# Performance work log

Measured on AMD Instinct MI355X. Metric: run time of the kernel, lower is better.

The kernel has to match this reference:

```python
import jax, jax.numpy as jnp
import numpy as np

A, B, K = 8192, 8192, 10

def setup_inputs() -> dict:
    key = jax.random.key(0)
    k1, k2, k3 = jax.random.split(key, 3)
    W = jax.random.uniform(k1, (A, B), dtype=jnp.float32)      # similarity weights (a,b)
    P_l = jax.random.uniform(k2, (A, K), dtype=jnp.float32)    # left cluster probs (a,k)
    P_r = jax.random.uniform(k3, (B, K), dtype=jnp.float32)    # right cluster probs (b,k)
    clusters_p = jnp.ones((K,), dtype=jnp.float32) / K         # nn.Parameter ones(k)/k
    return {"W": W, "P_l": P_l, "P_r": P_r, "clusters_p": clusters_p}

def reference(W, P_l, P_r, clusters_p):
    # Original math: sum_{a,b,k} W[a,b] * (P_l[a,k] + P_r[b,k] - 2*P_l[a,k]*P_r[b,k]) / clusters_p[k]
    # Decomposes exactly (no (a,b,k) intermediate):
    row_sum = W.sum(axis=1)                 # (a,)
    col_sum = W.sum(axis=0)                 # (b,)
    term_l = row_sum @ P_l                  # (k,)  sum_a rowsum[a] * P_l[a,k]
    term_r = col_sum @ P_r                  # (k,)  sum_b colsum[b] * P_r[b,k]
    WPr = W @ P_r                           # (a,k)
    cross = jnp.sum(P_l * WPr, axis=0)      # (k,)  diag(P_l^T W P_r)
    per_cluster = term_l + term_r - 2.0 * cross
    return jnp.sum(per_cluster / clusters_p)
```

## Files before the change

### kernel.cpp

```cpp
#include <hip/hip_runtime.h>


constexpr int K     = 10;
constexpr int TM    = 32;
constexpr int BLOCK = 256;
constexpr int TN    = BLOCK * 4;

__global__ void prcut_zero_out(float* out) {
    if (threadIdx.x == 0) out[0] = 0.0f;
}

__global__ __launch_bounds__(BLOCK) void prcut_main(
    const float* __restrict__ W,
    const float* __restrict__ Pl,
    const float* __restrict__ Pr,
    const float* __restrict__ cp,
    float* __restrict__ out,
    int Bn)
{
    float inv[K];
#pragma unroll
    for (int k = 0; k < K; ++k) inv[k] = 1.0f / cp[k];

    const int col4 = blockIdx.x * TN + threadIdx.x * 4;
    const int a0   = blockIdx.y * TM;

    float pr[4][K];
    float rs[4];
#pragma unroll
    for (int j = 0; j < 4; ++j) {
        const float* prp = Pr + (size_t)(col4 + j) * K;
        float s = 0.0f;
#pragma unroll
        for (int k = 0; k < K; ++k) {
            float v = prp[k] * inv[k];
            pr[j][k] = v;
            s += v;
        }
        rs[j] = s;
    }

    const float* wp = W + (size_t)a0 * Bn + col4;
    float acc = 0.0f;

#pragma unroll 4
    for (int r = 0; r < TM; ++r) {
        const float4 w = *reinterpret_cast<const float4*>(wp);
        wp += Bn;

        const float* plp = Pl + (size_t)(a0 + r) * K;
        float pl[K];
        float la = 0.0f;
#pragma unroll
        for (int k = 0; k < K; ++k) {
            pl[k] = plp[k];
            la = fmaf(pl[k], inv[k], la);
        }

        float d0 = 0.f, d1 = 0.f, d2 = 0.f, d3 = 0.f;
#pragma unroll
        for (int k = 0; k < K; ++k) {
            d0 = fmaf(pl[k], pr[0][k], d0);
            d1 = fmaf(pl[k], pr[1][k], d1);
            d2 = fmaf(pl[k], pr[2][k], d2);
            d3 = fmaf(pl[k], pr[3][k], d3);
        }

        const float c0 = fmaf(-2.0f, d0, la + rs[0]);
        const float c1 = fmaf(-2.0f, d1, la + rs[1]);
        const float c2 = fmaf(-2.0f, d2, la + rs[2]);
        const float c3 = fmaf(-2.0f, d3, la + rs[3]);

        acc = fmaf(w.x, c0, acc);
        acc = fmaf(w.y, c1, acc);
        acc = fmaf(w.z, c2, acc);
        acc = fmaf(w.w, c3, acc);
    }

#pragma unroll
    for (int off = 32; off > 0; off >>= 1)
        acc += __shfl_down(acc, off, 64);

    __shared__ float wsum[BLOCK / 64];
    const int lane = threadIdx.x & 63;
    const int wid  = threadIdx.x >> 6;
    if (lane == 0) wsum[wid] = acc;
    __syncthreads();

    if (threadIdx.x == 0) {
        float s = 0.0f;
#pragma unroll
        for (int i = 0; i < BLOCK / 64; ++i) s += wsum[i];
        atomicAdd(out, s);
    }
}

extern "C" void kernel_launch(void* const* d_in, const int* in_sizes, int n_in,
                              void* d_out, int out_size, void* d_ws, size_t ws_size,
                              hipStream_t stream) {
    const float* W  = (const float*)d_in[0];
    const float* Pl = (const float*)d_in[1];
    const float* Pr = (const float*)d_in[2];
    const float* cp = (const float*)d_in[3];
    float* out = (float*)d_out;

    const int Kn = in_sizes[3];
    const int A  = in_sizes[1] / Kn;
    const int B  = in_sizes[2] / Kn;

    prcut_zero_out<<<1, 64, 0, stream>>>(out);

    dim3 grid(B / TN, A / TM);
    prcut_main<<<grid, BLOCK, 0, stream>>>(W, Pl, Pr, cp, out, B);
}
```

Measured before the change: 378.8 us.

## Use full-row 1024-thread blocks with 8 columns per thread and nontemporal loads

Each block now covers a whole 16-row band of W, and each thread handles 8 columns split across the two halves of the row, so the Pr slices loaded into registers are reused across more W elements. The per-element coefficient is rewritten algebraically as la + sum_k pr_k*(1-2*pl_k), which drops the separate row-sum and the -2 fixups. W is read with nontemporal loads because it is streamed only once. Holding 80 pr values per thread in a 1024-thread block raises register pressure, and the grid is now one-dimensional with only 512 blocks, both of which can lower occupancy. The layout also assumes B equals 8*1024.

```diff
diff --git a/kernel.cpp b/kernel.cpp
--- a/kernel.cpp
+++ b/kernel.cpp
@@ -2,9 +2,10 @@
 
 
 constexpr int K     = 10;
-constexpr int TM    = 32;
-constexpr int BLOCK = 256;
-constexpr int TN    = BLOCK * 4;
+constexpr int TM    = 16;
+constexpr int BLOCK = 1024;
+
+typedef float f4 __attribute__((ext_vector_type(4)));
 
 __global__ void prcut_zero_out(float* out) {
     if (threadIdx.x == 0) out[0] = 0.0f;
@@ -22,59 +23,54 @@
 #pragma unroll
     for (int k = 0; k < K; ++k) inv[k] = 1.0f / cp[k];
 
-    const int col4 = blockIdx.x * TN + threadIdx.x * 4;
-    const int a0   = blockIdx.y * TM;
+    const int t    = threadIdx.x;
+    const int a0   = blockIdx.x * TM;
+    const int c0   = 4 * t;
+    const int half = Bn >> 1;
 
-    float pr[4][K];
-    float rs[4];
+    float pr[8][K];
 #pragma unroll
-    for (int j = 0; j < 4; ++j) {
-        const float* prp = Pr + (size_t)(col4 + j) * K;
-        float s = 0.0f;
+    for (int g = 0; g < 2; ++g) {
 #pragma unroll
-        for (int k = 0; k < K; ++k) {
-            float v = prp[k] * inv[k];
-            pr[j][k] = v;
-            s += v;
+        for (int j = 0; j < 4; ++j) {
+            const float* p = Pr + (size_t)(g * half + c0 + j) * K;
+#pragma unroll
+            for (int k = 0; k < K; ++k) pr[g * 4 + j][k] = p[k] * inv[k];
         }
-        rs[j] = s;
     }
 
-    const float* wp = W + (size_t)a0 * Bn + col4;
+    const float* wp = W + (size_t)a0 * Bn + c0;
     float acc = 0.0f;
 
-#pragma unroll 4
+#pragma unroll 2
     for (int r = 0; r < TM; ++r) {
-        const float4 w = *reinterpret_cast<const float4*>(wp);
+        const f4 w0 = __builtin_nontemporal_load(reinterpret_cast<const f4*>(wp));
+        const f4 w1 = __builtin_nontemporal_load(reinterpret_cast<const f4*>(wp + half));
         wp += Bn;
 
         const float* plp = Pl + (size_t)(a0 + r) * K;
-        float pl[K];
         float la = 0.0f;
+        float d[8];
+#pragma unroll
+        for (int j = 0; j < 8; ++j) d[j] = 0.0f;
+
 #pragma unroll
         for (int k = 0; k < K; ++k) {
-            pl[k] = plp[k];
-            la = fmaf(pl[k], inv[k], la);
+            const float plk = plp[k];
+            la = fmaf(plk, inv[k], la);
+            const float qk = fmaf(-2.0f, plk, 1.0f);
+#pragma unroll
+            for (int j = 0; j < 8; ++j) d[j] = fmaf(pr[j][k], qk, d[j]);
         }
 
-        float d0 = 0.f, d1 = 0.f, d2 = 0.f, d3 = 0.f;
-#pragma unroll
-        for (int k = 0; k < K; ++k) {
-            d0 = fmaf(pl[k], pr[0][k], d0);
-            d1 = fmaf(pl[k], pr[1][k], d1);
-            d2 = fmaf(pl[k], pr[2][k], d2);
-            d3 = fmaf(pl[k], pr[3][k], d3);
-        }
-
-        const float c0 = fmaf(-2.0f, d0, la + rs[0]);
-        const float c1 = fmaf(-2.0f, d1, la + rs[1]);
-        const float c2 = fmaf(-2.0f, d2, la + rs[2]);
-        const float c3 = fmaf(-2.0f, d3, la + rs[3]);
-
-        acc = fmaf(w.x, c0, acc);
-        acc = fmaf(w.y, c1, acc);
-        acc = fmaf(w.z, c2, acc);
-        acc = fmaf(w.w, c3, acc);
+        acc = fmaf(w0.x, la + d[0], acc);
+        acc = fmaf(w0.y, la + d[1], acc);
+        acc = fmaf(w0.z, la + d[2], acc);
+        acc = fmaf(w0.w, la + d[3], acc);
+        acc = fmaf(w1.x, la + d[4], acc);
+        acc = fmaf(w1.y, la + d[5], acc);
+        acc = fmaf(w1.z, la + d[6], acc);
+        acc = fmaf(w1.w, la + d[7], acc);
     }
 
 #pragma unroll
@@ -110,6 +106,5 @@
 
     prcut_zero_out<<<1, 64, 0, stream>>>(out);
 
-    dim3 grid(B / TN, A / TM);
-    prcut_main<<<grid, BLOCK, 0, stream>>>(W, Pl, Pr, cp, out, B);
+    prcut_main<<<A / TM, BLOCK, 0, stream>>>(W, Pl, Pr, cp, out, B);
 }
```

Result: faster. 367.1 us (-3.1%).

## Prefetch W rows in a register ring and widen blocks to half-row tiles

Applied to the files above, without the earlier changes.

Each block now spans half of a W row (1024 threads × 4 columns) with a grid of 2 × A/TM. A 4-deep register ring prefetches upcoming W rows so global loads overlap the per-row compute, and the final rows are drained in a separate epilogue loop. The goal is to hide memory latency on what is a bandwidth-bound streaming pass over W. In exchange it uses more registers and fewer, larger blocks, which may lower occupancy, and it hardcodes B/2 = 4096 columns per block.

```diff
diff --git a/kernel.cpp b/kernel.cpp
--- a/kernel.cpp
+++ b/kernel.cpp
@@ -3,8 +3,10 @@
 
 constexpr int K     = 10;
 constexpr int TM    = 32;
-constexpr int BLOCK = 256;
-constexpr int TN    = BLOCK * 4;
+constexpr int BLOCK = 1024;
+constexpr int P     = 4;
+
+typedef float f4 __attribute__((ext_vector_type(4)));
 
 __global__ void prcut_zero_out(float* out) {
     if (threadIdx.x == 0) out[0] = 0.0f;
@@ -22,59 +24,85 @@
 #pragma unroll
     for (int k = 0; k < K; ++k) inv[k] = 1.0f / cp[k];
 
-    const int col4 = blockIdx.x * TN + threadIdx.x * 4;
+    const int half = Bn >> 1;
+    const int c0   = blockIdx.x * half + threadIdx.x * 4;
     const int a0   = blockIdx.y * TM;
 
     float pr[4][K];
     float rs[4];
 #pragma unroll
     for (int j = 0; j < 4; ++j) {
-        const float* prp = Pr + (size_t)(col4 + j) * K;
+        const float* p = Pr + (size_t)(c0 + j) * K;
         float s = 0.0f;
 #pragma unroll
         for (int k = 0; k < K; ++k) {
-            float v = prp[k] * inv[k];
+            float v = p[k] * inv[k];
             pr[j][k] = v;
             s += v;
         }
         rs[j] = s;
     }
 
-    const float* wp = W + (size_t)a0 * Bn + col4;
+    const float* wp  = W + (size_t)a0 * Bn + c0;
+    const float* wld = wp + (size_t)P * Bn;
+
+    f4 wbuf[P];
+#pragma unroll
+    for (int i = 0; i < P; ++i)
+        wbuf[i] = *reinterpret_cast<const f4*>(wp + (size_t)i * Bn);
+
     float acc = 0.0f;
 
 #pragma unroll 4
-    for (int r = 0; r < TM; ++r) {
-        const float4 w = *reinterpret_cast<const float4*>(wp);
-        wp += Bn;
-
+    for (int r = 0; r < TM - P; ++r) {
         const float* plp = Pl + (size_t)(a0 + r) * K;
-        float pl[K];
         float la = 0.0f;
 #pragma unroll
-        for (int k = 0; k < K; ++k) {
-            pl[k] = plp[k];
-            la = fmaf(pl[k], inv[k], la);
-        }
+        for (int k = 0; k < K; ++k) la = fmaf(plp[k], inv[k], la);
 
         float d0 = 0.f, d1 = 0.f, d2 = 0.f, d3 = 0.f;
 #pragma unroll
         for (int k = 0; k < K; ++k) {
-            d0 = fmaf(pl[k], pr[0][k], d0);
-            d1 = fmaf(pl[k], pr[1][k], d1);
-            d2 = fmaf(pl[k], pr[2][k], d2);
-            d3 = fmaf(pl[k], pr[3][k], d3);
+            const float plk = plp[k];
+            d0 = fmaf(plk, pr[0][k], d0);
+            d1 = fmaf(plk, pr[1][k], d1);
+            d2 = fmaf(plk, pr[2][k], d2);
+            d3 = fmaf(plk, pr[3][k], d3);
         }
 
-        const float c0 = fmaf(-2.0f, d0, la + rs[0]);
-        const float c1 = fmaf(-2.0f, d1, la + rs[1]);
-        const float c2 = fmaf(-2.0f, d2, la + rs[2]);
-        const float c3 = fmaf(-2.0f, d3, la + rs[3]);
+        const int slot = r & (P - 1);
+        const f4 w = wbuf[slot];
+        wbuf[slot] = *reinterpret_cast<const f4*>(wld);
+        wld += Bn;
 
-        acc = fmaf(w.x, c0, acc);
-        acc = fmaf(w.y, c1, acc);
-        acc = fmaf(w.z, c2, acc);
-        acc = fmaf(w.w, c3, acc);
+        acc = fmaf(w.x, fmaf(-2.0f, d0, la + rs[0]), acc);
+        acc = fmaf(w.y, fmaf(-2.0f, d1, la + rs[1]), acc);
+        acc = fmaf(w.z, fmaf(-2.0f, d2, la + rs[2]), acc);
+        acc = fmaf(w.w, fmaf(-2.0f, d3, la + rs[3]), acc);
+    }
+
+#pragma unroll
+    for (int r = TM - P; r < TM; ++r) {
+        const float* plp = Pl + (size_t)(a0 + r) * K;
+        float la = 0.0f;
+#pragma unroll
+        for (int k = 0; k < K; ++k) la = fmaf(plp[k], inv[k], la);
+
+        float d0 = 0.f, d1 = 0.f, d2 = 0.f, d3 = 0.f;
+#pragma unroll
+        for (int k = 0; k < K; ++k) {
+            const float plk = plp[k];
+            d0 = fmaf(plk, pr[0][k], d0);
+            d1 = fmaf(plk, pr[1][k], d1);
+            d2 = fmaf(plk, pr[2][k], d2);
+            d3 = fmaf(plk, pr[3][k], d3);
+        }
+
+        const f4 w = wbuf[r & (P - 1)];
+        acc = fmaf(w.x, fmaf(-2.0f, d0, la + rs[0]), acc);
+        acc = fmaf(w.y, fmaf(-2.0f, d1, la + rs[1]), acc);
+        acc = fmaf(w.z, fmaf(-2.0f, d2, la + rs[2]), acc);
+        acc = fmaf(w.w, fmaf(-2.0f, d3, la + rs[3]), acc);
     }
 
 #pragma unroll
@@ -110,6 +138,6 @@
 
     prcut_zero_out<<<1, 64, 0, stream>>>(out);
 
-    dim3 grid(B / TN, A / TM);
+    dim3 grid(2, A / TM);
     prcut_main<<<grid, BLOCK, 0, stream>>>(W, Pl, Pr, cp, out, B);
 }
```

Result: faster. 362.4 us (-4.3%).
